# Kernel tuning notes

Hardware: AMD Instinct MI355X
Metric: run time of the kernel (lower is better)

## Reference

```python
import jax, jax.numpy as jnp
import numpy as np

ALPHA, BETA, GAMMA = 1.0, 1.0, 0.001
DELTA_V, DELTA_D = 0.5, 1.5
NORM = 2


def _lp_norm(x, p, axis):
    # grad-safe Lp norm: avoids d/dx sqrt(0) NaNs on exactly-zero rows (diagonal pairs)
    ss = jnp.sum(jnp.abs(x) ** p, axis=axis)
    safe = jnp.where(ss > 0, ss, 1.0)
    return jnp.where(ss > 0, safe ** (1.0 / p), 0.0)


def setup_inputs() -> dict:
    key = jax.random.key(0)
    k1, k2, k3 = jax.random.split(key, 3)
    bs, n_filters, H, W, n_inst = 8, 16, 128, 128, 24
    inp = jax.random.normal(k1, (bs, n_filters, H, W), dtype=jnp.float32)
    target = jax.random.randint(k2, (bs, n_inst, H, W), 0, 2).astype(jnp.int32)
    # every sample has at least 2 objects so dist term is exercised and no 0/0
    n_objects = jax.random.randint(k3, (bs, 1), 2, n_inst + 1).astype(jnp.int32)
    return {"input": inp, "target": target, "n_objects": n_objects, "max_n_objects": n_inst}


def reference(input, target, n_objects, max_n_objects):
    bs, n_filters, H, W = input.shape
    n_inst = target.shape[1]
    L = H * W
    pred = jnp.transpose(input, (0, 2, 3, 1)).reshape(bs, L, n_filters)  # (bs, L, F)
    gt = jnp.transpose(target, (0, 2, 3, 1)).reshape(bs, L, n_inst).astype(jnp.float32)  # (bs, L, I)

    nobj = n_objects[:, 0]  # (bs,)
    nf = nobj.astype(jnp.float32)
    valid = (jnp.arange(n_inst)[None, :] < nobj[:, None]).astype(jnp.float32)  # (bs, I)
    gt_m = gt * valid[:, None, :]

    # cluster means: masked sum / masked count, zero-filled past n_objects
    counts = gt_m.sum(axis=1)  # (bs, I)
    sums = jnp.einsum('bli,blf->bif', gt_m, pred)  # (bs, I, F)
    means = jnp.where((valid > 0)[..., None],
                      sums / jnp.where(counts > 0, counts, 1.0)[..., None], 0.0)

    # variance term
    dn = _lp_norm(pred[:, :, None, :] - means[:, None, :, :], NORM, 3)  # (bs, L, I)
    var = jnp.maximum(dn - DELTA_V, 0.0) ** 2 * gt
    var_num = jnp.sum(var * valid[:, None, :], axis=(1, 2))
    var_den = jnp.sum(gt_m, axis=(1, 2))
    var_term = jnp.mean(var_num / var_den)

    # distance term (pairwise hinge over valid instance pairs)
    mdn = _lp_norm(means[:, :, None, :] - means[:, None, :, :], NORM, 3)  # (bs, I, I)
    margin = 2.0 * DELTA_D * (1.0 - jnp.eye(n_inst, dtype=jnp.float32))[None]
    pair_mask = valid[:, :, None] * valid[:, None, :]
    hinge = jnp.maximum(margin - mdn, 0.0) ** 2 * pair_mask
    denom = jnp.where(nf > 1, nf * (nf - 1.0), 1.0)
    per_sample = jnp.where(nf > 1, jnp.sum(hinge, axis=(1, 2)) / denom, 0.0)
    dist_term = jnp.mean(per_sample)

    # regularization term
    row_norms = _lp_norm(means, NORM, 2)  # (bs, I)
    reg_term = jnp.mean(jnp.sum(row_norms * valid, axis=1) / nf)

    return ALPHA * var_term + BETA * dist_term + GAMMA * reg_term
```

## Files before the change

### kernel.cpp

```cpp
#include <hip/hip_runtime.h>

#define BS 8
#define NF 16
#define NI 24
#define LL 16384

#define NCH 64
#define CPX (LL/NCH)
#define RBLK 32
#define RTH 512
#define I_PER 3

#define OFF_PSUMS 0
#define OFF_PCNTS (BS*NCH*NI*NF)
#define OFF_VNUM  (OFF_PCNTS + BS*NCH*NI)
#define OFF_VDEN  (OFF_VNUM + BS)
#define OFF_DIST  (OFF_VDEN + BS)
#define OFF_REG   (OFF_DIST + BS)
#define OFF_DONE  (OFF_REG + BS)

__device__ __forceinline__ float wave_sum63(float v) {
    v += __int_as_float(__builtin_amdgcn_update_dpp(0, __float_as_int(v), 0x111, 0xf, 0xf, true));
    v += __int_as_float(__builtin_amdgcn_update_dpp(0, __float_as_int(v), 0x112, 0xf, 0xf, true));
    v += __int_as_float(__builtin_amdgcn_update_dpp(0, __float_as_int(v), 0x114, 0xf, 0xf, true));
    v += __int_as_float(__builtin_amdgcn_update_dpp(0, __float_as_int(v), 0x118, 0xf, 0xf, true));
    v += __int_as_float(__builtin_amdgcn_update_dpp(0, __float_as_int(v), 0x142, 0xa, 0xf, true));
    v += __int_as_float(__builtin_amdgcn_update_dpp(0, __float_as_int(v), 0x143, 0xc, 0xf, true));
    return v;
}

__device__ __forceinline__ float block_sum(float v, volatile float* red) {
    for (int off = 32; off; off >>= 1) v += __shfl_down(v, off);
    __syncthreads();
    if ((threadIdx.x & 63) == 0) red[threadIdx.x >> 6] = v;
    __syncthreads();
    float r = 0.f;
    int nw = blockDim.x >> 6;
    if ((int)threadIdx.x < nw) r = red[threadIdx.x];
    if ((threadIdx.x >> 6) == 0)
        for (int off = 32; off; off >>= 1) r += __shfl_down(r, off);
    return r;
}

__global__ __launch_bounds__(512, 4) void k_sums(const float* __restrict__ input,
                                                 const int* __restrict__ target,
                                                 float* __restrict__ ws) {
    const int b    = blockIdx.y;
    const int c    = blockIdx.x;
    const int w    = threadIdx.x >> 6;
    const int lane = threadIdx.x & 63;
    const int i0   = w * I_PER;
    const int l    = c * CPX + lane * 4;
    const float* inb = input + (size_t)b * NF * LL;
    const int*   tgb = target + (size_t)b * NI * LL;

    float tvf[I_PER][4];
    #pragma unroll
    for (int ii = 0; ii < I_PER; ++ii) {
        int4 tv = *reinterpret_cast<const int4*>(tgb + (i0 + ii) * LL + l);
        tvf[ii][0] = (float)tv.x; tvf[ii][1] = (float)tv.y;
        tvf[ii][2] = (float)tv.z; tvf[ii][3] = (float)tv.w;
    }
    float acc[I_PER][NF];
    float cnt[I_PER];
    #pragma unroll
    for (int ii = 0; ii < I_PER; ++ii) {
        cnt[ii] = (tvf[ii][0] + tvf[ii][1]) + (tvf[ii][2] + tvf[ii][3]);
        #pragma unroll
        for (int f = 0; f < NF; ++f) acc[ii][f] = 0.f;
    }
    #pragma unroll
    for (int f = 0; f < NF; ++f) {
        float4 p = *reinterpret_cast<const float4*>(inb + f * LL + l);
        #pragma unroll
        for (int ii = 0; ii < I_PER; ++ii) {
            float a = acc[ii][f];
            a = fmaf(tvf[ii][0], p.x, a);
            a = fmaf(tvf[ii][1], p.y, a);
            a = fmaf(tvf[ii][2], p.z, a);
            a = fmaf(tvf[ii][3], p.w, a);
            acc[ii][f] = a;
        }
    }

    #pragma unroll
    for (int ii = 0; ii < I_PER; ++ii) {
        #pragma unroll
        for (int f = 0; f < NF; ++f) acc[ii][f] = wave_sum63(acc[ii][f]);
        cnt[ii] = wave_sum63(cnt[ii]);
    }
    if (lane == 63) {
        float* ps = ws + OFF_PSUMS + (((size_t)b * NCH + c) * NI + i0) * NF;
        float* pc = ws + OFF_PCNTS + ((size_t)b * NCH + c) * NI + i0;
        #pragma unroll
        for (int ii = 0; ii < I_PER; ++ii) {
            #pragma unroll
            for (int f = 0; f < NF; ++f) ps[ii * NF + f] = acc[ii][f];
            pc[ii] = cnt[ii];
        }
    }
    if (c == 0 && threadIdx.x == 0) {
        ws[OFF_VNUM + b] = 0.f;
        if (b == 0) *(int*)(ws + OFF_DONE) = 0;
    }
}

__global__ __launch_bounds__(512, 4) void k_rest(const float* __restrict__ input,
                                                 const int* __restrict__ target,
                                                 const int* __restrict__ n_objects,
                                                 float* __restrict__ ws,
                                                 float* __restrict__ out) {
    const int b = blockIdx.y;
    const int t = threadIdx.x;
    const int n = n_objects[b];
    __shared__ float m_lds[NI][NF];
    __shared__ float c_lds[NI];
    __shared__ float red[8];
    __shared__ int amLast;

    float rawsum = 0.f;
    if (t < NI * NF) {
        const float* ps = ws + OFF_PSUMS + (size_t)b * NCH * NI * NF + t;
        #pragma unroll 8
        for (int c = 0; c < NCH; ++c) rawsum += ps[(size_t)c * NI * NF];
    } else if (t >= NI * NF && t < NI * NF + NI) {
        const float* pc = ws + OFF_PCNTS + (size_t)b * NCH * NI + (t - NI * NF);
        float s = 0.f;
        #pragma unroll 8
        for (int c = 0; c < NCH; ++c) s += pc[c * NI];
        c_lds[t - NI * NF] = s;
    }
    __syncthreads();
    if (t < NI * NF) {
        int i = t >> 4;
        float cv = c_lds[i];
        m_lds[i][t & 15] = (i < n) ? rawsum / (cv > 0.f ? cv : 1.f) : 0.f;
    }
    __syncthreads();

    const float* inb = input + (size_t)b * NF * LL;
    const int*   tgb = target + (size_t)b * NI * LL;
    const int l = blockIdx.x * RTH + t;
    float p[NF];
    #pragma unroll
    for (int f = 0; f < NF; ++f) p[f] = inb[f * LL + l];
    float acc = 0.f;
    for (int i = 0; i < n; ++i) {
        float tv = (float)tgb[i * LL + l];
        float ss = 0.f;
        #pragma unroll
        for (int f = 0; f < NF; ++f) { float d = p[f] - m_lds[i][f]; ss = fmaf(d, d, ss); }
        float h = fmaxf(sqrtf(ss) - 0.5f, 0.f);
        acc = fmaf(tv, h * h, acc);
    }
    float vsum = block_sum(acc, red);

    if (blockIdx.x == 0) {
        float vden = 0.f, reg = 0.f;
        if (t < NI && t < n) {
            vden = c_lds[t];
            float ss = 0.f;
            #pragma unroll
            for (int f = 0; f < NF; ++f) { float m = m_lds[t][f]; ss += m * m; }
            reg = (ss > 0.f) ? sqrtf(ss) : 0.f;
        }
        float dist = 0.f;
        for (int pp = t; pp < NI * NI; pp += RTH) {
            int i = pp / NI, j = pp % NI;
            if (i != j && i < n && j < n) {
                float ss = 0.f;
                #pragma unroll
                for (int f = 0; f < NF; ++f) { float d = m_lds[i][f] - m_lds[j][f]; ss += d * d; }
                float dn = (ss > 0.f) ? sqrtf(ss) : 0.f;
                float h = fmaxf(3.0f - dn, 0.f);
                dist += h * h;
            }
        }
        float vden_s = block_sum(vden, red);
        float reg_s  = block_sum(reg, red);
        float dist_s = block_sum(dist, red);
        if (t == 0) {
            float nf = (float)n;
            __hip_atomic_store(&ws[OFF_VDEN + b], vden_s, __ATOMIC_RELAXED, __HIP_MEMORY_SCOPE_AGENT);
            __hip_atomic_store(&ws[OFF_REG + b], reg_s / nf, __ATOMIC_RELAXED, __HIP_MEMORY_SCOPE_AGENT);
            __hip_atomic_store(&ws[OFF_DIST + b],
                               (n > 1) ? dist_s / (nf * (nf - 1.f)) : 0.f,
                               __ATOMIC_RELAXED, __HIP_MEMORY_SCOPE_AGENT);
        }
    }

    if (t == 0) {
        atomicAdd(&ws[OFF_VNUM + b], vsum);
        __threadfence();
        int prev = atomicAdd((int*)(ws + OFF_DONE), 1);
        amLast = (prev == RBLK * BS - 1) ? 1 : 0;
    }
    __syncthreads();
    if (amLast && t == 0) {
        __threadfence();
        float total = 0.f;
        for (int b2 = 0; b2 < BS; ++b2) {
            float vn = __hip_atomic_load(&ws[OFF_VNUM + b2], __ATOMIC_RELAXED, __HIP_MEMORY_SCOPE_AGENT);
            float vd = __hip_atomic_load(&ws[OFF_VDEN + b2], __ATOMIC_RELAXED, __HIP_MEMORY_SCOPE_AGENT);
            float dt = __hip_atomic_load(&ws[OFF_DIST + b2], __ATOMIC_RELAXED, __HIP_MEMORY_SCOPE_AGENT);
            float rg = __hip_atomic_load(&ws[OFF_REG + b2], __ATOMIC_RELAXED, __HIP_MEMORY_SCOPE_AGENT);
            total += vn / vd + dt + 0.001f * rg;
        }
        out[0] = total * (1.0f / (float)BS);
    }
}

extern "C" void kernel_launch(void* const* d_in, const int* in_sizes, int n_in,
                              void* d_out, int out_size, void* d_ws, size_t ws_size,
                              hipStream_t stream) {
    const float* input     = (const float*)d_in[0];
    const int*   target    = (const int*)d_in[1];
    const int*   n_objects = (const int*)d_in[2];
    float* ws  = (float*)d_ws;
    float* out = (float*)d_out;

    dim3 gA(NCH, BS);
    k_sums<<<gA, 512, 0, stream>>>(input, target, ws);
    dim3 gB(RBLK, BS);
    k_rest<<<gB, 512, 0, stream>>>(input, target, n_objects, ws, out);
}
```

Before: 91.32 us.

## Fuse sums and variance kernels into one cooperative kernel with grid syncs

```diff
diff --git a/kernel.cpp b/kernel.cpp
--- a/kernel.cpp
+++ b/kernel.cpp
@@ -1,14 +1,15 @@
 #include <hip/hip_runtime.h>
+#include <hip/hip_cooperative_groups.h>
+
+namespace cg = cooperative_groups;
 
 #define BS 8
 #define NF 16
 #define NI 24
 #define LL 16384
 
-#define NCH 64
+#define NCH 32
 #define CPX (LL/NCH)
-#define RBLK 32
-#define RTH 512
 #define I_PER 3
 
 #define OFF_PSUMS 0
@@ -17,7 +18,6 @@
 #define OFF_VDEN  (OFF_VNUM + BS)
 #define OFF_DIST  (OFF_VDEN + BS)
 #define OFF_REG   (OFF_DIST + BS)
-#define OFF_DONE  (OFF_REG + BS)
 
 __device__ __forceinline__ float wave_sum63(float v) {
     v += __int_as_float(__builtin_amdgcn_update_dpp(0, __float_as_int(v), 0x111, 0xf, 0xf, true));
@@ -42,120 +42,122 @@
     return r;
 }
 
-__global__ __launch_bounds__(512, 4) void k_sums(const float* __restrict__ input,
-                                                 const int* __restrict__ target,
-                                                 float* __restrict__ ws) {
-    const int b    = blockIdx.y;
-    const int c    = blockIdx.x;
-    const int w    = threadIdx.x >> 6;
-    const int lane = threadIdx.x & 63;
-    const int i0   = w * I_PER;
-    const int l    = c * CPX + lane * 4;
+__global__ __launch_bounds__(512, 2) void k_fused(const float* __restrict__ input,
+                                                  const int* __restrict__ target,
+                                                  const int* __restrict__ n_objects,
+                                                  float* __restrict__ ws,
+                                                  float* __restrict__ out) {
+    cg::grid_group grid = cg::this_grid();
+    const int b    = blockIdx.x >> 5;
+    const int c    = blockIdx.x & (NCH - 1);
+    const int t    = threadIdx.x;
+    const int w    = t >> 6;
+    const int lane = t & 63;
     const float* inb = input + (size_t)b * NF * LL;
     const int*   tgb = target + (size_t)b * NI * LL;
 
-    float tvf[I_PER][4];
-    #pragma unroll
-    for (int ii = 0; ii < I_PER; ++ii) {
-        int4 tv = *reinterpret_cast<const int4*>(tgb + (i0 + ii) * LL + l);
-        tvf[ii][0] = (float)tv.x; tvf[ii][1] = (float)tv.y;
-        tvf[ii][2] = (float)tv.z; tvf[ii][3] = (float)tv.w;
-    }
-    float acc[I_PER][NF];
-    float cnt[I_PER];
-    #pragma unroll
-    for (int ii = 0; ii < I_PER; ++ii) {
-        cnt[ii] = (tvf[ii][0] + tvf[ii][1]) + (tvf[ii][2] + tvf[ii][3]);
-        #pragma unroll
-        for (int f = 0; f < NF; ++f) acc[ii][f] = 0.f;
-    }
-    #pragma unroll
-    for (int f = 0; f < NF; ++f) {
-        float4 p = *reinterpret_cast<const float4*>(inb + f * LL + l);
+    {
+        const int i0 = w * I_PER;
+        float acc[I_PER][NF];
+        float cnt[I_PER];
         #pragma unroll
         for (int ii = 0; ii < I_PER; ++ii) {
-            float a = acc[ii][f];
-            a = fmaf(tvf[ii][0], p.x, a);
-            a = fmaf(tvf[ii][1], p.y, a);
-            a = fmaf(tvf[ii][2], p.z, a);
-            a = fmaf(tvf[ii][3], p.w, a);
-            acc[ii][f] = a;
-        }
-    }
-
-    #pragma unroll
-    for (int ii = 0; ii < I_PER; ++ii) {
-        #pragma unroll
-        for (int f = 0; f < NF; ++f) acc[ii][f] = wave_sum63(acc[ii][f]);
-        cnt[ii] = wave_sum63(cnt[ii]);
-    }
-    if (lane == 63) {
-        float* ps = ws + OFF_PSUMS + (((size_t)b * NCH + c) * NI + i0) * NF;
-        float* pc = ws + OFF_PCNTS + ((size_t)b * NCH + c) * NI + i0;
+            cnt[ii] = 0.f;
+            #pragma unroll
+            for (int f = 0; f < NF; ++f) acc[ii][f] = 0.f;
+        }
+        #pragma unroll
+        for (int step = 0; step < CPX / 256; ++step) {
+            const int l = c * CPX + step * 256 + lane * 4;
+            float tvf[I_PER][4];
+            #pragma unroll
+            for (int ii = 0; ii < I_PER; ++ii) {
+                int4 tv = *reinterpret_cast<const int4*>(tgb + (i0 + ii) * LL + l);
+                tvf[ii][0] = (float)tv.x; tvf[ii][1] = (float)tv.y;
+                tvf[ii][2] = (float)tv.z; tvf[ii][3] = (float)tv.w;
+                cnt[ii] += (tvf[ii][0] + tvf[ii][1]) + (tvf[ii][2] + tvf[ii][3]);
+            }
+            #pragma unroll
+            for (int f = 0; f < NF; ++f) {
+                float4 p = *reinterpret_cast<const float4*>(inb + f * LL + l);
+                #pragma unroll
+                for (int ii = 0; ii < I_PER; ++ii) {
+                    float a = acc[ii][f];
+                    a = fmaf(tvf[ii][0], p.x, a);
+                    a = fmaf(tvf[ii][1], p.y, a);
+                    a = fmaf(tvf[ii][2], p.z, a);
+                    a = fmaf(tvf[ii][3], p.w, a);
+                    acc[ii][f] = a;
+                }
+            }
+        }
         #pragma unroll
         for (int ii = 0; ii < I_PER; ++ii) {
             #pragma unroll
-            for (int f = 0; f < NF; ++f) ps[ii * NF + f] = acc[ii][f];
-            pc[ii] = cnt[ii];
-        }
-    }
-    if (c == 0 && threadIdx.x == 0) {
-        ws[OFF_VNUM + b] = 0.f;
-        if (b == 0) *(int*)(ws + OFF_DONE) = 0;
-    }
-}
-
-__global__ __launch_bounds__(512, 4) void k_rest(const float* __restrict__ input,
-                                                 const int* __restrict__ target,
-                                                 const int* __restrict__ n_objects,
-                                                 float* __restrict__ ws,
-                                                 float* __restrict__ out) {
-    const int b = blockIdx.y;
-    const int t = threadIdx.x;
+            for (int f = 0; f < NF; ++f) acc[ii][f] = wave_sum63(acc[ii][f]);
+            cnt[ii] = wave_sum63(cnt[ii]);
+        }
+        if (lane == 63) {
+            float* ps = ws + OFF_PSUMS + (((size_t)b * NCH + c) * NI + i0) * NF;
+            float* pc = ws + OFF_PCNTS + ((size_t)b * NCH + c) * NI + i0;
+            #pragma unroll
+            for (int ii = 0; ii < I_PER; ++ii) {
+                #pragma unroll
+                for (int f = 0; f < NF; ++f) ps[ii * NF + f] = acc[ii][f];
+                pc[ii] = cnt[ii];
+            }
+        }
+        if (c == 0 && t == 0) ws[OFF_VNUM + b] = 0.f;
+    }
+
+    grid.sync();
+
     const int n = n_objects[b];
     __shared__ float m_lds[NI][NF];
     __shared__ float c_lds[NI];
     __shared__ float red[8];
-    __shared__ int amLast;
-
-    float rawsum = 0.f;
-    if (t < NI * NF) {
-        const float* ps = ws + OFF_PSUMS + (size_t)b * NCH * NI * NF + t;
-        #pragma unroll 8
-        for (int c = 0; c < NCH; ++c) rawsum += ps[(size_t)c * NI * NF];
-    } else if (t >= NI * NF && t < NI * NF + NI) {
-        const float* pc = ws + OFF_PCNTS + (size_t)b * NCH * NI + (t - NI * NF);
-        float s = 0.f;
-        #pragma unroll 8
-        for (int c = 0; c < NCH; ++c) s += pc[c * NI];
-        c_lds[t - NI * NF] = s;
-    }
-    __syncthreads();
-    if (t < NI * NF) {
-        int i = t >> 4;
-        float cv = c_lds[i];
-        m_lds[i][t & 15] = (i < n) ? rawsum / (cv > 0.f ? cv : 1.f) : 0.f;
-    }
-    __syncthreads();
-
-    const float* inb = input + (size_t)b * NF * LL;
-    const int*   tgb = target + (size_t)b * NI * LL;
-    const int l = blockIdx.x * RTH + t;
-    float p[NF];
-    #pragma unroll
-    for (int f = 0; f < NF; ++f) p[f] = inb[f * LL + l];
-    float acc = 0.f;
-    for (int i = 0; i < n; ++i) {
-        float tv = (float)tgb[i * LL + l];
-        float ss = 0.f;
-        #pragma unroll
-        for (int f = 0; f < NF; ++f) { float d = p[f] - m_lds[i][f]; ss = fmaf(d, d, ss); }
-        float h = fmaxf(sqrtf(ss) - 0.5f, 0.f);
-        acc = fmaf(tv, h * h, acc);
-    }
-    float vsum = block_sum(acc, red);
-
-    if (blockIdx.x == 0) {
+
+    {
+        float rawsum = 0.f;
+        if (t < NI * NF) {
+            const float* ps = ws + OFF_PSUMS + (size_t)b * NCH * NI * NF + t;
+            #pragma unroll 8
+            for (int cc = 0; cc < NCH; ++cc) rawsum += ps[(size_t)cc * NI * NF];
+        } else if (t < NI * NF + NI) {
+            const float* pc = ws + OFF_PCNTS + (size_t)b * NCH * NI + (t - NI * NF);
+            float s = 0.f;
+            #pragma unroll 8
+            for (int cc = 0; cc < NCH; ++cc) s += pc[cc * NI];
+            c_lds[t - NI * NF] = s;
+        }
+        __syncthreads();
+        if (t < NI * NF) {
+            int i = t >> 4;
+            float cv = c_lds[i];
+            m_lds[i][t & 15] = (i < n) ? rawsum / (cv > 0.f ? cv : 1.f) : 0.f;
+        }
+        __syncthreads();
+    }
+
+    {
+        const int l = c * CPX + t;
+        float p[NF];
+        #pragma unroll
+        for (int f = 0; f < NF; ++f) p[f] = inb[f * LL + l];
+        float acc = 0.f;
+        for (int i = 0; i < n; ++i) {
+            float tv = (float)tgb[i * LL + l];
+            float ss = 0.f;
+            #pragma unroll
+            for (int f = 0; f < NF; ++f) { float d = p[f] - m_lds[i][f]; ss = fmaf(d, d, ss); }
+            float h = fmaxf(sqrtf(ss) - 0.5f, 0.f);
+            acc = fmaf(tv, h * h, acc);
+        }
+        float vsum = block_sum(acc, red);
+        if (t == 0) atomicAdd(&ws[OFF_VNUM + b], vsum);
+    }
+
+    if (c == 0) {
         float vden = 0.f, reg = 0.f;
         if (t < NI && t < n) {
             vden = c_lds[t];
@@ -165,7 +167,7 @@
             reg = (ss > 0.f) ? sqrtf(ss) : 0.f;
         }
         float dist = 0.f;
-        for (int pp = t; pp < NI * NI; pp += RTH) {
+        for (int pp = t; pp < NI * NI; pp += 512) {
             int i = pp / NI, j = pp % NI;
             if (i != j && i < n && j < n) {
                 float ss = 0.f;
@@ -181,30 +183,20 @@
         float dist_s = block_sum(dist, red);
         if (t == 0) {
             float nf = (float)n;
-            __hip_atomic_store(&ws[OFF_VDEN + b], vden_s, __ATOMIC_RELAXED, __HIP_MEMORY_SCOPE_AGENT);
-            __hip_atomic_store(&ws[OFF_REG + b], reg_s / nf, __ATOMIC_RELAXED, __HIP_MEMORY_SCOPE_AGENT);
-            __hip_atomic_store(&ws[OFF_DIST + b],
-                               (n > 1) ? dist_s / (nf * (nf - 1.f)) : 0.f,
-                               __ATOMIC_RELAXED, __HIP_MEMORY_SCOPE_AGENT);
-        }
-    }
-
-    if (t == 0) {
-        atomicAdd(&ws[OFF_VNUM + b], vsum);
-        __threadfence();
-        int prev = atomicAdd((int*)(ws + OFF_DONE), 1);
-        amLast = (prev == RBLK * BS - 1) ? 1 : 0;
-    }
-    __syncthreads();
-    if (amLast && t == 0) {
-        __threadfence();
+            ws[OFF_VDEN + b] = vden_s;
+            ws[OFF_REG + b]  = reg_s / nf;
+            ws[OFF_DIST + b] = (n > 1) ? dist_s / (nf * (nf - 1.f)) : 0.f;
+        }
+    }
+
+    grid.sync();
+
+    if (blockIdx.x == 0 && t == 0) {
         float total = 0.f;
         for (int b2 = 0; b2 < BS; ++b2) {
-            float vn = __hip_atomic_load(&ws[OFF_VNUM + b2], __ATOMIC_RELAXED, __HIP_MEMORY_SCOPE_AGENT);
-            float vd = __hip_atomic_load(&ws[OFF_VDEN + b2], __ATOMIC_RELAXED, __HIP_MEMORY_SCOPE_AGENT);
-            float dt = __hip_atomic_load(&ws[OFF_DIST + b2], __ATOMIC_RELAXED, __HIP_MEMORY_SCOPE_AGENT);
-            float rg = __hip_atomic_load(&ws[OFF_REG + b2], __ATOMIC_RELAXED, __HIP_MEMORY_SCOPE_AGENT);
-            total += vn / vd + dt + 0.001f * rg;
+            total += ws[OFF_VNUM + b2] / ws[OFF_VDEN + b2]
+                   + ws[OFF_DIST + b2]
+                   + 0.001f * ws[OFF_REG + b2];
         }
         out[0] = total * (1.0f / (float)BS);
     }
@@ -219,8 +211,7 @@
     float* ws  = (float*)d_ws;
     float* out = (float*)d_out;
 
-    dim3 gA(NCH, BS);
-    k_sums<<<gA, 512, 0, stream>>>(input, target, ws);
-    dim3 gB(RBLK, BS);
-    k_rest<<<gB, 512, 0, stream>>>(input, target, n_objects, ws, out);
-}
+    void* args[] = {(void*)&input, (void*)&target, (void*)&n_objects, (void*)&ws, (void*)&out};
+    hipLaunchCooperativeKernel((const void*)k_fused, dim3(BS * NCH), dim3(512),
+                               args, 0, stream);
+}
```

Result: slower. 146.6 us (+60.5%).
